# Kernel optimization log

Hardware: AMD Instinct MI355X
Metric: run time of the kernel (lower is better)

## Reference

```python
import jax, jax.numpy as jnp
import numpy as np

DIM = 512
HEADS = 8
HEAD = DIM // HEADS
T = 243          # temporal length, fixed by get_temporal_mask(243, ...)
N_JOINTS = 17    # skeleton joints
BATCH = 4        # number of clips; leading dim of x is BATCH*T
WINDOWS = (9, 27, 81, 243)  # temporal_MoE_type


def _temporal_masks():
    # Block-diagonal window masks: 0 inside each window block, -100000 outside,
    # exactly matching get_temporal_mask + torch.where(matrix == 0, -100000, 0).
    idx = np.arange(T)
    masks = np.stack([
        np.where((idx[:, None] // w) == (idx[None, :] // w), 0.0, -100000.0)
        for w in WINDOWS
    ]).astype(np.float32)  # (E, T, T)
    return jnp.asarray(masks)


def setup_inputs() -> dict:
    key = jax.random.key(0)
    k0, k1, k2, k3 = jax.random.split(key, 4)
    scaled = lambda k, shape, fan: jax.random.normal(k, shape, jnp.float32) * (fan ** -0.5)
    return {
        "x": jax.random.normal(k0, (BATCH * T, N_JOINTS, DIM), jnp.float32),
        "qkv_w": scaled(k1, (DIM, 3 * DIM), DIM),          # qkv (no bias, qkv_bias=False)
        "proj_w": scaled(k2, (DIM, DIM), DIM),             # output projection
        "proj_b": jnp.zeros((DIM,), jnp.float32),
        "te_w": scaled(k3, (DIM, len(WINDOWS)), DIM),      # temporal_expert_linear
        "te_b": jnp.zeros((len(WINDOWS),), jnp.float32),
        "seqlen": T,
    }


def reference(x, qkv_w, proj_w, proj_b, te_w, te_b, seqlen):
    BT, n, C = x.shape              # (b*T, N, C)
    b = BT // seqlen
    scale = HEAD ** -0.5
    # qkv projection -> q,k,v each (b, H, N, T, head_dim)
    qkv = (x @ qkv_w).reshape(b, seqlen, n, 3, HEADS, HEAD)
    qkv = jnp.transpose(qkv, (3, 0, 4, 2, 1, 5))  # (3, b, H, N, T, c)
    q, k, v = qkv[0], qkv[1], qkv[2]
    # temporal attention logits, shared across experts: (b, H, N, T, T)
    attn = jnp.einsum('bhntc,bhnsc->bhnts', q, k) * scale
    masks = _temporal_masks()                       # (E, T, T)
    attn = attn[None] + masks[:, None, None, None]  # (E, b, H, N, T, T)
    attn = jax.nn.softmax(attn, axis=-1)            # attn_drop is identity (p=0 / eval)
    eo = jnp.einsum('ebhnts,bhnsc->ebhntc', attn, v)
    E = masks.shape[0]
    # (E,b,H,N,T,c) -> (E,b,T,N,H,c) -> (E, b*T, N, C), matching permute(0,3,2,1,4)
    eo = jnp.transpose(eo, (0, 1, 4, 3, 2, 5)).reshape(E, BT, n, C)
    # expert gating: softmax(temporal_expert_linear(x)) over experts, per token
    w = jax.nn.softmax(x @ te_w + te_b, axis=-1)    # (BT, N, E)
    out = jnp.einsum('ebnc,bne->bnc', eo, w)        # fused expert recombination
    out = out @ proj_w + proj_b                     # proj (proj_drop identity)
    return out
```

## Files before the change

kernel.cpp:

```cpp
#include <hip/hip_runtime.h>
#include <hip/hip_bf16.h>
#include <cstdint>

#define TT 243
#define NJ 17
#define NB 4
#define NH 8
#define HD 64
#define CDIM 512
#define NROWS (NB*TT*NJ)
#define NBHN (NB*NH*NJ)

typedef unsigned short u16;
typedef __attribute__((ext_vector_type(8))) short short8;
typedef __attribute__((ext_vector_type(4))) float f32x4;

#define MFMA16(a, b, c) __builtin_amdgcn_mfma_f32_16x16x32_bf16((a), (b), (c), 0, 0, 0)
#define QSCALE 0.18033688011112042f

__device__ __forceinline__ void gl_lds16(const void* g, void* l) {
  __builtin_amdgcn_global_load_lds(
      (const __attribute__((address_space(1))) void*)g,
      (__attribute__((address_space(3))) void*)l, 16, 0, 0);
}

__device__ __forceinline__ u16 f2bf(float f) {
  union { float f; unsigned u; } v; v.f = f;
  unsigned r = v.u + 0x7FFFu + ((v.u >> 16) & 1u);
  return (u16)(r >> 16);
}

__device__ __forceinline__ float fast_exp2(float x) {
#if __has_builtin(__builtin_amdgcn_exp2f)
  return __builtin_amdgcn_exp2f(x);
#else
  return exp2f(x);
#endif
}
__device__ __forceinline__ float fast_rcp(float x) {
#if __has_builtin(__builtin_amdgcn_rcpf)
  return __builtin_amdgcn_rcpf(x);
#else
  return 1.f / x;
#endif
}
__device__ __forceinline__ unsigned pk_bf16(float a, float b) {
#if __has_builtin(__builtin_amdgcn_cvt_pk_bf16_f32)
  auto pk = __builtin_amdgcn_cvt_pk_bf16_f32(a, b);
  unsigned u; __builtin_memcpy(&u, &pk, sizeof(u));
  return u;
#else
  return (unsigned)f2bf(a) | ((unsigned)f2bf(b) << 16);
#endif
}

__device__ __forceinline__ float wave_reduce_sum(float v) {
#pragma unroll
  for (int off = 32; off > 0; off >>= 1) v += __shfl_xor(v, off, 64);
  return v;
}

#define CG_BLOCKS ((NROWS + 3) / 4)
#define T1_NB 48
#define T1_BLOCKS (48 * 16)
#define T2_NB 16
#define T2_BLOCKS (16 * 16)

__device__ __forceinline__ void trans_body(const float* __restrict__ in,
                                           u16* __restrict__ out, int K, int N,
                                           int nb, int kb, float (*tile)[33]) {
  int n0 = nb * 32, k0 = kb * 32;
  int tx = threadIdx.x & 31, ty = threadIdx.x >> 5;
#pragma unroll
  for (int p = 0; p < 4; ++p)
    tile[ty + p * 8][tx] = in[(size_t)(k0 + ty + p * 8) * N + n0 + tx];
  __syncthreads();
#pragma unroll
  for (int p = 0; p < 4; ++p)
    out[(size_t)(n0 + ty + p * 8) * K + k0 + tx] = f2bf(tile[tx][ty + p * 8]);
}

__global__ __launch_bounds__(256) void prep_kernel(
    const float* __restrict__ x, const float* __restrict__ te_w,
    const float* __restrict__ te_b, const float* __restrict__ qkv_w,
    const float* __restrict__ proj_w, u16* __restrict__ xb,
    float* __restrict__ gates, u16* __restrict__ wt, u16* __restrict__ pwt) {
  __shared__ float tile[32][33];
  int bid = blockIdx.x;
  if (bid >= CG_BLOCKS) {
    int r = bid - CG_BLOCKS;
    if (r < T1_BLOCKS) trans_body(qkv_w, wt, 512, 1536, r % T1_NB, r / T1_NB, tile);
    else {
      r -= T1_BLOCKS;
      trans_body(proj_w, pwt, 512, 512, r % T2_NB, r / T2_NB, tile);
    }
    return;
  }
  int w = threadIdx.x >> 6, l = threadIdx.x & 63;
  int row = bid * 4 + w;
  if (row >= NROWS) return;
  const float* xr = x + (size_t)row * CDIM;
  u16* xo = xb + (size_t)row * CDIM;
  float a0 = 0.f, a1 = 0.f, a2 = 0.f, a3 = 0.f;
#pragma unroll
  for (int p = 0; p < 2; ++p) {
    int c = (p * 64 + l) * 4;
    float4 v = *(const float4*)(xr + c);
    uint2 o;
    o.x = pk_bf16(v.x, v.y);
    o.y = pk_bf16(v.z, v.w);
    *(uint2*)(xo + c) = o;
    float xv[4] = {v.x, v.y, v.z, v.w};
#pragma unroll
    for (int q = 0; q < 4; ++q) {
      float4 wv = *(const float4*)(te_w + (size_t)(c + q) * 4);
      a0 += xv[q] * wv.x; a1 += xv[q] * wv.y;
      a2 += xv[q] * wv.z; a3 += xv[q] * wv.w;
    }
  }
  a0 = wave_reduce_sum(a0);
  a1 = wave_reduce_sum(a1);
  a2 = wave_reduce_sum(a2);
  a3 = wave_reduce_sum(a3);
  a0 += te_b[0]; a1 += te_b[1]; a2 += te_b[2]; a3 += te_b[3];
  float mx = fmaxf(fmaxf(a0, a1), fmaxf(a2, a3));
  float e0 = __expf(a0 - mx), e1 = __expf(a1 - mx);
  float e2 = __expf(a2 - mx), e3 = __expf(a3 - mx);
  float inv = fast_rcp(e0 + e1 + e2 + e3);
  if (l == 0) {
    *(float4*)(gates + (size_t)row * 4) =
        make_float4(e0 * inv, e1 * inv, e2 * inv, e3 * inv);
  }
}

__global__ __launch_bounds__(256) void qkv_gemm(
    const u16* __restrict__ xb, const u16* __restrict__ wt,
    u16* __restrict__ qh, u16* __restrict__ kh, u16* __restrict__ vb) {
  __shared__ u16 S[16640];
  u16* Al = S;
  u16* Bl = S + 8192;
  int tid = threadIdx.x;
  int w = tid >> 6;
  int c16 = tid & 15, g4 = (tid >> 4) & 3;
  int r0 = blockIdx.y * 128, n0 = blockIdx.x * 128;
  int wm = w & 1, wn = w >> 1;

  int rA = tid >> 3;
  int c8off = (((tid & 7) ^ (rA & 7)) * 8);
  size_t arow4[4], brow4[4];
#pragma unroll
  for (int it = 0; it < 4; ++it) {
    int m = r0 + it * 32 + rA;
    if (m >= NROWS) m = NROWS - 1;
    int bj = m / 243, t = m - bj * 243;
    int b = bj / 17, j = bj - b * 17;
    arow4[it] = ((size_t)(b * 243 + t) * 17 + j) * 512;
    brow4[it] = (size_t)(n0 + it * 32 + rA) * 512;
  }

  f32x4 acc[4][4] = {};
  for (int k0 = 0; k0 < CDIM; k0 += 64) {
    __syncthreads();
#pragma unroll
    for (int it = 0; it < 4; ++it) {
      gl_lds16(xb + arow4[it] + k0 + c8off, Al + (size_t)(it * 256 + (w * 64)) * 8);
      gl_lds16(wt + brow4[it] + k0 + c8off, Bl + (size_t)(it * 256 + (w * 64)) * 8);
    }
    __syncthreads();
    short8 af[4][2], bf[4][2];
#pragma unroll
    for (int i = 0; i < 4; ++i) {
      int rowa = wm * 64 + i * 16 + c16;
#pragma unroll
      for (int hh = 0; hh < 2; ++hh)
        af[i][hh] = *(const short8*)(Al + rowa * 64 + (((hh * 4 + g4) ^ (c16 & 7)) * 8));
    }
#pragma unroll
    for (int j = 0; j < 4; ++j) {
      int rowb = wn * 64 + j * 16 + c16;
#pragma unroll
      for (int hh = 0; hh < 2; ++hh)
        bf[j][hh] = *(const short8*)(Bl + rowb * 64 + (((hh * 4 + g4) ^ (c16 & 7)) * 8));
    }
#pragma unroll
    for (int i = 0; i < 4; ++i)
#pragma unroll
      for (int j = 0; j < 4; ++j) {
        acc[i][j] = MFMA16(af[i][0], bf[j][0], acc[i][j]);
        acc[i][j] = MFMA16(af[i][1], bf[j][1], acc[i][j]);
      }
  }

  if (n0 < 1024) {
#pragma unroll
    for (int i = 0; i < 4; ++i)
#pragma unroll
      for (int r = 0; r < 4; ++r) {
        int m = r0 + wm * 64 + i * 16 + g4 * 4 + r;
        if (m >= NROWS) continue;
        int bj = m / 243, t = m - bj * 243;
        int b = bj / 17, j = bj - b * 17;
#pragma unroll
        for (int jt = 0; jt < 4; ++jt) {
          int col = n0 + wn * 64 + jt * 16 + c16;
          int sel = col >> 9, h = (col >> 6) & 7, c = col & 63;
          u16* dst = sel ? kh : qh;
          float val = acc[i][jt][r];
          if (!sel) val *= QSCALE;
          dst[((size_t)((b * 8 + h) * 17 + j) * 243 + t) * 64 + c] = f2bf(val);
        }
      }
  } else {
    __syncthreads();
#pragma unroll
    for (int i = 0; i < 4; ++i)
#pragma unroll
      for (int jt = 0; jt < 4; ++jt)
#pragma unroll
        for (int r = 0; r < 4; ++r) {
          int row = wm * 64 + i * 16 + g4 * 4 + r;
          int colI = wn * 64 + jt * 16 + c16;
          S[colI * 130 + row] = f2bf(acc[i][jt][r]);
        }
    __syncthreads();
    int l = tid & 63;
    int hb = (n0 - 1024) >> 6;
    int m0 = r0 + 2 * l;
    int m1 = m0 + 1;
    bool v0 = m0 < NROWS, v1 = m1 < NROWS;
    int bj0 = m0 / 243, t0 = m0 - bj0 * 243;
    int b0 = bj0 / 17, j0 = bj0 - b0 * 17;
    int bj1 = m1 / 243, t1 = m1 - bj1 * 243;
    int b1 = bj1 / 17, j1 = bj1 - b1 * 17;
    size_t base0 = ((size_t)(b0 * 136 + j0) * 64) * 256 + t0;
    size_t base1 = ((size_t)(b1 * 136 + j1) * 64) * 256 + t1;
#pragma unroll 8
    for (int cc = 0; cc < 32; ++cc) {
      int colI = w * 32 + cc;
      int h = hb + (colI >> 6), c = colI & 63;
      ushort2 u = *(const ushort2*)&S[colI * 130 + 2 * l];
      size_t hoff = ((size_t)h * 17 * 64) * 256 + (size_t)c * 256;
      if (v0) vb[base0 + hoff] = u.x;
      if (v1) vb[base1 + hoff] = u.y;
    }
  }
}

__global__ __launch_bounds__(256, 4) void attn_kernel(
    const u16* __restrict__ qh, const u16* __restrict__ kh,
    const u16* __restrict__ vb, const float* __restrict__ gates,
    u16* __restrict__ preb) {
  __shared__ u16 L[16384];
  int bhn = blockIdx.x;
  int q0 = blockIdx.y * 64;
  int b = bhn / (NH * NJ);
  int hj = bhn - b * (NH * NJ);
  int h = hj / NJ, j = hj - h * NJ;
  int tid = threadIdx.x;
  int w = tid >> 6;
  int c16 = tid & 15, g4 = (tid >> 4) & 3;
  const u16* Kp = kh + (size_t)bhn * (TT * HD);
  const u16* Qp = qh + (size_t)bhn * (TT * HD);
  const u16* Vp = vb + (size_t)bhn * (HD * 256);
  u16* Rw = L + w * 4096;

#pragma unroll
  for (int it = 0; it < 8; ++it) {
    int F = it * 256 + tid;
    int s = F >> 3;
    int c8 = (F & 7) ^ (s & 7);
    int sg = s < TT ? s : TT - 1;
    gl_lds16(Kp + (size_t)sg * 64 + c8 * 8, L + (size_t)(it * 256 + (tid & ~63)) * 8);
  }
  __syncthreads();

  int tt = q0 + w * 16 + c16;
  bool tvalid = tt < TT;
  int tg = tvalid ? tt : TT - 1;

  short8 bq[2];
#pragma unroll
  for (int hh = 0; hh < 2; ++hh)
    bq[hh] = *(const short8*)(Qp + (size_t)tg * 64 + hh * 32 + g4 * 8);

  f32x4 acc[16];
#pragma unroll
  for (int st = 0; st < 16; ++st) acc[st] = (f32x4)(0.f);
#pragma unroll
  for (int st = 0; st < 16; ++st) {
    int sf = st * 16 + c16;
#pragma unroll
    for (int hh = 0; hh < 2; ++hh) {
      short8 ak = *(const short8*)(L + sf * 64 + ((hh * 4 + g4) ^ (sf & 7)) * 8);
      acc[st] = MFMA16(ak, bq[hh], acc[st]);
    }
  }
  __syncthreads();

#pragma unroll
  for (int r = 0; r < 4; ++r) {
    int s = 240 + g4 * 4 + r;
    if (s >= TT) acc[15][r] = -1e30f;
  }
  float M = -1e30f;
#pragma unroll
  for (int st = 0; st < 16; ++st)
#pragma unroll
    for (int r = 0; r < 4; ++r) M = fmaxf(M, acc[st][r]);
  M = fmaxf(M, __shfl_xor(M, 16, 64));
  M = fmaxf(M, __shfl_xor(M, 32, 64));

#pragma unroll
  for (int st = 0; st < 16; ++st)
#pragma unroll
    for (int r = 0; r < 4; ++r) acc[st][r] = fast_exp2(acc[st][r] - M);

  int t9b = (tg / 9) * 9;
  int t27b = (tg / 27) * 27;
  int t81b = (tg / 81) * 81;
  float l9 = 0.f, l27 = 0.f, l81 = 0.f, l243 = 0.f;
#pragma unroll
  for (int st = 0; st < 16; ++st)
#pragma unroll
    for (int r = 0; r < 4; ++r) {
      int s = st * 16 + g4 * 4 + r;
      float e = acc[st][r];
      l243 += e;
      l81 += ((unsigned)(s - t81b) < 81u) ? e : 0.f;
      l27 += ((unsigned)(s - t27b) < 27u) ? e : 0.f;
      l9  += ((unsigned)(s - t9b)  <  9u) ? e : 0.f;
    }
  l9   += __shfl_xor(l9, 16, 64);   l9   += __shfl_xor(l9, 32, 64);
  l27  += __shfl_xor(l27, 16, 64);  l27  += __shfl_xor(l27, 32, 64);
  l81  += __shfl_xor(l81, 16, 64);  l81  += __shfl_xor(l81, 32, 64);
  l243 += __shfl_xor(l243, 16, 64); l243 += __shfl_xor(l243, 32, 64);

  float4 gv = *(const float4*)(gates + ((size_t)(b * TT + tg) * NJ + j) * 4);
  float gam3 = gv.w * fast_rcp(l243);
  float gam2 = gam3 + gv.z * fast_rcp(l81);
  float gam1 = gam2 + gv.y * fast_rcp(l27);
  float gam0 = gam1 + gv.x * fast_rcp(l9);

#pragma unroll
  for (int st = 0; st < 16; ++st) {
    float rv[4];
#pragma unroll
    for (int r = 0; r < 4; ++r) {
      int s = st * 16 + g4 * 4 + r;
      float e = acc[st][r];
      float cw = ((unsigned)(s - t9b) < 9u) ? gam0
               : ((unsigned)(s - t27b) < 27u) ? gam1
               : ((unsigned)(s - t81b) < 81u) ? gam2 : gam3;
      rv[r] = tvalid ? e * cw : 0.f;
    }
    uint2 pk;
    pk.x = pk_bf16(rv[0], rv[1]);
    pk.y = pk_bf16(rv[2], rv[3]);
    int c8 = st * 2 + (g4 >> 1);
    int slot = (c8 & 24) | ((c8 & 7) ^ (c16 & 7));
    *(uint2*)(Rw + c16 * 256 + slot * 8 + (g4 & 1) * 4) = pk;
  }

  short8 ar[8];
#pragma unroll
  for (int h2 = 0; h2 < 8; ++h2) {
    int cc = h2 * 4 + g4;
    int slot = (cc & 24) | ((cc & 7) ^ (c16 & 7));
    ar[h2] = *(const short8*)(Rw + c16 * 256 + slot * 8);
  }
#pragma unroll
  for (int jt = 0; jt < 4; ++jt) {
    int c = jt * 16 + c16;
    f32x4 o = (f32x4)(0.f);
#pragma unroll
    for (int h2 = 0; h2 < 8; ++h2) {
      short8 bv = *(const short8*)(Vp + (size_t)c * 256 + h2 * 32 + g4 * 8);
      o = MFMA16(ar[h2], bv, o);
    }
#pragma unroll
    for (int r = 0; r < 4; ++r) {
      int t = q0 + w * 16 + g4 * 4 + r;
      if (t < TT)
        preb[((size_t)(b * TT + t) * NJ + j) * 512 + h * 64 + c] = f2bf(o[r]);
    }
  }
}

__global__ __launch_bounds__(256) void proj_gemm(
    const u16* __restrict__ preb, const u16* __restrict__ pwt,
    const float* __restrict__ bias, float* __restrict__ out) {
  __shared__ u16 Al[8192];
  __shared__ u16 Bl[8192];
  int tid = threadIdx.x;
  int w = tid >> 6;
  int c16 = tid & 15, g4 = (tid >> 4) & 3;
  int r0 = blockIdx.y * 128, n0 = blockIdx.x * 128;
  int wm = w & 1, wn = w >> 1;

  int rA = tid >> 3;
  int c8off = (((tid & 7) ^ (rA & 7)) * 8);
  size_t arow4[4], brow4[4];
#pragma unroll
  for (int it = 0; it < 4; ++it) {
    int m = r0 + it * 32 + rA;
    if (m >= NROWS) m = NROWS - 1;
    arow4[it] = (size_t)m * 512;
    brow4[it] = (size_t)(n0 + it * 32 + rA) * 512;
  }

  f32x4 acc[4][4] = {};
  for (int k0 = 0; k0 < CDIM; k0 += 64) {
    __syncthreads();
#pragma unroll
    for (int it = 0; it < 4; ++it) {
      gl_lds16(preb + arow4[it] + k0 + c8off, Al + (size_t)(it * 256 + (w * 64)) * 8);
      gl_lds16(pwt + brow4[it] + k0 + c8off, Bl + (size_t)(it * 256 + (w * 64)) * 8);
    }
    __syncthreads();
    short8 af[4][2], bf[4][2];
#pragma unroll
    for (int i = 0; i < 4; ++i) {
      int rowa = wm * 64 + i * 16 + c16;
#pragma unroll
      for (int hh = 0; hh < 2; ++hh)
        af[i][hh] = *(const short8*)(Al + rowa * 64 + (((hh * 4 + g4) ^ (c16 & 7)) * 8));
    }
#pragma unroll
    for (int j = 0; j < 4; ++j) {
      int rowb = wn * 64 + j * 16 + c16;
#pragma unroll
      for (int hh = 0; hh < 2; ++hh)
        bf[j][hh] = *(const short8*)(Bl + rowb * 64 + (((hh * 4 + g4) ^ (c16 & 7)) * 8));
    }
#pragma unroll
    for (int i = 0; i < 4; ++i)
#pragma unroll
      for (int j = 0; j < 4; ++j) {
        acc[i][j] = MFMA16(af[i][0], bf[j][0], acc[i][j]);
        acc[i][j] = MFMA16(af[i][1], bf[j][1], acc[i][j]);
      }
  }
#pragma unroll
  for (int i = 0; i < 4; ++i)
#pragma unroll
    for (int r = 0; r < 4; ++r) {
      int row = r0 + wm * 64 + i * 16 + g4 * 4 + r;
      if (row >= NROWS) continue;
#pragma unroll
      for (int jt = 0; jt < 4; ++jt) {
        int col = n0 + wn * 64 + jt * 16 + c16;
        out[(size_t)row * 512 + col] = acc[i][jt][r] + bias[col];
      }
    }
}

extern "C" void kernel_launch(void* const* d_in, const int* in_sizes, int n_in,
                              void* d_out, int out_size, void* d_ws, size_t ws_size,
                              hipStream_t stream) {
  (void)in_sizes; (void)n_in; (void)out_size; (void)ws_size;
  const float* x      = (const float*)d_in[0];
  const float* qkv_w  = (const float*)d_in[1];
  const float* proj_w = (const float*)d_in[2];
  const float* proj_b = (const float*)d_in[3];
  const float* te_w   = (const float*)d_in[4];
  const float* te_b   = (const float*)d_in[5];

  char* p = (char*)d_ws;
  auto alloc = [&](size_t bytes) {
    void* r = (void*)p;
    p += (bytes + 255) & ~(size_t)255;
    return r;
  };
  u16*   xb    = (u16*)alloc((size_t)NROWS * 512 * 2);
  u16*   wt    = (u16*)alloc((size_t)1536 * 512 * 2);
  u16*   pwt   = (u16*)alloc((size_t)512 * 512 * 2);
  float* gates = (float*)alloc((size_t)NROWS * 4 * 4);
  u16*   qhb   = (u16*)alloc((size_t)NBHN * 243 * 64 * 2);
  u16*   khb   = (u16*)alloc((size_t)NBHN * 243 * 64 * 2);
  u16*   vb    = (u16*)alloc((size_t)NBHN * 64 * 256 * 2);
  u16*   preb  = (u16*)alloc((size_t)NROWS * 512 * 2);
  float* out   = (float*)d_out;

  hipLaunchKernelGGL(prep_kernel, dim3(CG_BLOCKS + T1_BLOCKS + T2_BLOCKS), dim3(256),
                     0, stream, x, te_w, te_b, qkv_w, proj_w, xb, gates, wt, pwt);
  hipLaunchKernelGGL(qkv_gemm, dim3(12, (NROWS + 127) / 128), dim3(256), 0, stream,
                     xb, wt, qhb, khb, vb);
  hipLaunchKernelGGL(attn_kernel, dim3(NBHN, 4), dim3(256), 0, stream,
                     qhb, khb, vb, gates, preb);
  hipLaunchKernelGGL(proj_gemm, dim3(4, (NROWS + 127) / 128), dim3(256), 0, stream,
                     preb, pwt, proj_b, out);
}
```

Measured before the change: 213.5 us.

## Fuse x bf16 conversion and expert gating into QKV GEMM

Removes the separate pass that converts x to bf16 and computes the gating softmax. The QKV GEMM now loads fp32 x directly, converts it in registers and writes it into LDS, and an extra column of blocks computes the gate logits with MFMA against a transposed bf16 te_w. The attention softmax sums are restructured to accumulate in vectors, and the invalid-row masking is folded into the gamma coefficients. In exchange, every GEMM block re-reads fp32 x, which doubles its A-side traffic and loses the async LDS loads, and the gate logits are now computed in bf16.

```diff
diff --git a/kernel.cpp b/kernel.cpp
--- a/kernel.cpp
+++ b/kernel.cpp
@@ -54,13 +54,6 @@
 #endif
 }
 
-__device__ __forceinline__ float wave_reduce_sum(float v) {
-#pragma unroll
-  for (int off = 32; off > 0; off >>= 1) v += __shfl_xor(v, off, 64);
-  return v;
-}
-
-#define CG_BLOCKS ((NROWS + 3) / 4)
 #define T1_NB 48
 #define T1_BLOCKS (48 * 16)
 #define T2_NB 16
@@ -81,73 +74,43 @@
 }
 
 __global__ __launch_bounds__(256) void prep_kernel(
-    const float* __restrict__ x, const float* __restrict__ te_w,
-    const float* __restrict__ te_b, const float* __restrict__ qkv_w,
-    const float* __restrict__ proj_w, u16* __restrict__ xb,
-    float* __restrict__ gates, u16* __restrict__ wt, u16* __restrict__ pwt) {
+    const float* __restrict__ qkv_w, const float* __restrict__ proj_w,
+    const float* __restrict__ te_w, u16* __restrict__ wt,
+    u16* __restrict__ pwt, u16* __restrict__ tewt) {
   __shared__ float tile[32][33];
   int bid = blockIdx.x;
-  if (bid >= CG_BLOCKS) {
-    int r = bid - CG_BLOCKS;
-    if (r < T1_BLOCKS) trans_body(qkv_w, wt, 512, 1536, r % T1_NB, r / T1_NB, tile);
-    else {
-      r -= T1_BLOCKS;
-      trans_body(proj_w, pwt, 512, 512, r % T2_NB, r / T2_NB, tile);
-    }
-    return;
-  }
-  int w = threadIdx.x >> 6, l = threadIdx.x & 63;
-  int row = bid * 4 + w;
-  if (row >= NROWS) return;
-  const float* xr = x + (size_t)row * CDIM;
-  u16* xo = xb + (size_t)row * CDIM;
-  float a0 = 0.f, a1 = 0.f, a2 = 0.f, a3 = 0.f;
-#pragma unroll
-  for (int p = 0; p < 2; ++p) {
-    int c = (p * 64 + l) * 4;
-    float4 v = *(const float4*)(xr + c);
-    uint2 o;
-    o.x = pk_bf16(v.x, v.y);
-    o.y = pk_bf16(v.z, v.w);
-    *(uint2*)(xo + c) = o;
-    float xv[4] = {v.x, v.y, v.z, v.w};
-#pragma unroll
-    for (int q = 0; q < 4; ++q) {
-      float4 wv = *(const float4*)(te_w + (size_t)(c + q) * 4);
-      a0 += xv[q] * wv.x; a1 += xv[q] * wv.y;
-      a2 += xv[q] * wv.z; a3 += xv[q] * wv.w;
-    }
-  }
-  a0 = wave_reduce_sum(a0);
-  a1 = wave_reduce_sum(a1);
-  a2 = wave_reduce_sum(a2);
-  a3 = wave_reduce_sum(a3);
-  a0 += te_b[0]; a1 += te_b[1]; a2 += te_b[2]; a3 += te_b[3];
-  float mx = fmaxf(fmaxf(a0, a1), fmaxf(a2, a3));
-  float e0 = __expf(a0 - mx), e1 = __expf(a1 - mx);
-  float e2 = __expf(a2 - mx), e3 = __expf(a3 - mx);
-  float inv = fast_rcp(e0 + e1 + e2 + e3);
-  if (l == 0) {
-    *(float4*)(gates + (size_t)row * 4) =
-        make_float4(e0 * inv, e1 * inv, e2 * inv, e3 * inv);
+  if (bid < T1_BLOCKS) {
+    trans_body(qkv_w, wt, 512, 1536, bid % T1_NB, bid / T1_NB, tile);
+  } else if (bid < T1_BLOCKS + T2_BLOCKS) {
+    int r = bid - T1_BLOCKS;
+    trans_body(proj_w, pwt, 512, 512, r % T2_NB, r / T2_NB, tile);
+  } else {
+#pragma unroll
+    for (int i = 0; i < 8; ++i) {
+      int idx = threadIdx.x + i * 256;
+      int e = idx >> 9, c = idx & 511;
+      tewt[idx] = f2bf(te_w[(size_t)c * 4 + e]);
+    }
   }
 }
 
 __global__ __launch_bounds__(256) void qkv_gemm(
-    const u16* __restrict__ xb, const u16* __restrict__ wt,
-    u16* __restrict__ qh, u16* __restrict__ kh, u16* __restrict__ vb) {
+    const float* __restrict__ xf, const u16* __restrict__ wt,
+    const u16* __restrict__ tewt, const float* __restrict__ te_b,
+    u16* __restrict__ qh, u16* __restrict__ kh, u16* __restrict__ vb,
+    float* __restrict__ gates) {
   __shared__ u16 S[16640];
   u16* Al = S;
   u16* Bl = S + 8192;
   int tid = threadIdx.x;
   int w = tid >> 6;
   int c16 = tid & 15, g4 = (tid >> 4) & 3;
-  int r0 = blockIdx.y * 128, n0 = blockIdx.x * 128;
-  int wm = w & 1, wn = w >> 1;
-
+  int r0 = blockIdx.y * 128;
+  int bx = blockIdx.x;
   int rA = tid >> 3;
-  int c8off = (((tid & 7) ^ (rA & 7)) * 8);
-  size_t arow4[4], brow4[4];
+  int c8e = (((tid & 7) ^ (rA & 7)) * 8);
+
+  size_t arow4[4];
 #pragma unroll
   for (int it = 0; it < 4; ++it) {
     int m = r0 + it * 32 + rA;
@@ -155,16 +118,97 @@
     int bj = m / 243, t = m - bj * 243;
     int b = bj / 17, j = bj - b * 17;
     arow4[it] = ((size_t)(b * 243 + t) * 17 + j) * 512;
+  }
+
+  if (bx == 12) {
+    u16* Tl = Bl;
+    *(uint2*)(Tl + tid * 4) = make_uint2(0u, 0u);
+    f32x4 gacc[2] = {};
+    for (int k0 = 0; k0 < CDIM; k0 += 64) {
+      __syncthreads();
+      float4 fa[4][2];
+#pragma unroll
+      for (int it = 0; it < 4; ++it) {
+        const float* src = xf + arow4[it] + k0 + c8e;
+        fa[it][0] = *(const float4*)(src);
+        fa[it][1] = *(const float4*)(src + 4);
+      }
+#pragma unroll
+      for (int it = 0; it < 4; ++it) {
+        uint4 pkv;
+        pkv.x = pk_bf16(fa[it][0].x, fa[it][0].y);
+        pkv.y = pk_bf16(fa[it][0].z, fa[it][0].w);
+        pkv.z = pk_bf16(fa[it][1].x, fa[it][1].y);
+        pkv.w = pk_bf16(fa[it][1].z, fa[it][1].w);
+        *(uint4*)(Al + (size_t)(it * 256 + tid) * 8) = pkv;
+      }
+      if (tid < 32) {
+        int row = tid >> 3;
+        gl_lds16(tewt + (size_t)row * 512 + k0 + (((tid & 7) ^ row) * 8), Tl);
+      }
+      __syncthreads();
+      short8 tf[2];
+#pragma unroll
+      for (int hh = 0; hh < 2; ++hh)
+        tf[hh] = *(const short8*)(Tl + c16 * 64 + (((hh * 4 + g4) ^ (c16 & 7)) * 8));
+#pragma unroll
+      for (int i2 = 0; i2 < 2; ++i2) {
+        int rowa = w * 32 + i2 * 16 + c16;
+#pragma unroll
+        for (int hh = 0; hh < 2; ++hh) {
+          short8 af = *(const short8*)(Al + rowa * 64 + (((hh * 4 + g4) ^ (c16 & 7)) * 8));
+          gacc[i2] = MFMA16(af, tf[hh], gacc[i2]);
+        }
+      }
+    }
+    float bias = (c16 < 4) ? te_b[c16 & 3] : 0.f;
+#pragma unroll
+    for (int i2 = 0; i2 < 2; ++i2)
+#pragma unroll
+      for (int r = 0; r < 4; ++r) {
+        int m = r0 + w * 32 + i2 * 16 + g4 * 4 + r;
+        if (m >= NROWS) continue;
+        float v = gacc[i2][r] + bias;
+        float mx = fmaxf(v, __shfl_xor(v, 1, 64));
+        mx = fmaxf(mx, __shfl_xor(mx, 2, 64));
+        float e = __expf(v - mx);
+        float sum = e + __shfl_xor(e, 1, 64);
+        sum += __shfl_xor(sum, 2, 64);
+        if (c16 < 4) {
+          int bj = m / 243, t = m - bj * 243;
+          int b = bj / 17, j = bj - b * 17;
+          gates[((size_t)(b * 243 + t) * 17 + j) * 4 + c16] = e * fast_rcp(sum);
+        }
+      }
+    return;
+  }
+
+  int n0 = bx * 128;
+  int wm = w & 1, wn = w >> 1;
+  size_t brow4[4];
+#pragma unroll
+  for (int it = 0; it < 4; ++it)
     brow4[it] = (size_t)(n0 + it * 32 + rA) * 512;
-  }
 
   f32x4 acc[4][4] = {};
   for (int k0 = 0; k0 < CDIM; k0 += 64) {
     __syncthreads();
+    float4 fa[4][2];
 #pragma unroll
     for (int it = 0; it < 4; ++it) {
-      gl_lds16(xb + arow4[it] + k0 + c8off, Al + (size_t)(it * 256 + (w * 64)) * 8);
-      gl_lds16(wt + brow4[it] + k0 + c8off, Bl + (size_t)(it * 256 + (w * 64)) * 8);
+      const float* src = xf + arow4[it] + k0 + c8e;
+      fa[it][0] = *(const float4*)(src);
+      fa[it][1] = *(const float4*)(src + 4);
+    }
+#pragma unroll
+    for (int it = 0; it < 4; ++it) {
+      gl_lds16(wt + brow4[it] + k0 + c8e, Bl + (size_t)(it * 256 + (w * 64)) * 8);
+      uint4 pkv;
+      pkv.x = pk_bf16(fa[it][0].x, fa[it][0].y);
+      pkv.y = pk_bf16(fa[it][0].z, fa[it][0].w);
+      pkv.z = pk_bf16(fa[it][1].x, fa[it][1].y);
+      pkv.w = pk_bf16(fa[it][1].z, fa[it][1].w);
+      *(uint4*)(Al + (size_t)(it * 256 + tid) * 8) = pkv;
     }
     __syncthreads();
     short8 af[4][2], bf[4][2];
@@ -318,18 +362,24 @@
   int t9b = (tg / 9) * 9;
   int t27b = (tg / 27) * 27;
   int t81b = (tg / 81) * 81;
-  float l9 = 0.f, l27 = 0.f, l81 = 0.f, l243 = 0.f;
+  f32x4 vall = acc[0];
+#pragma unroll
+  for (int st = 1; st < 16; ++st) vall += acc[st];
+  float l243 = (vall[0] + vall[1]) + (vall[2] + vall[3]);
+  f32x4 v81 = (f32x4)(0.f), v27 = (f32x4)(0.f), v9 = (f32x4)(0.f);
 #pragma unroll
   for (int st = 0; st < 16; ++st)
 #pragma unroll
     for (int r = 0; r < 4; ++r) {
       int s = st * 16 + g4 * 4 + r;
       float e = acc[st][r];
-      l243 += e;
-      l81 += ((unsigned)(s - t81b) < 81u) ? e : 0.f;
-      l27 += ((unsigned)(s - t27b) < 27u) ? e : 0.f;
-      l9  += ((unsigned)(s - t9b)  <  9u) ? e : 0.f;
-    }
+      v81[r] += ((unsigned)(s - t81b) < 81u) ? e : 0.f;
+      v27[r] += ((unsigned)(s - t27b) < 27u) ? e : 0.f;
+      v9[r]  += ((unsigned)(s - t9b)  <  9u) ? e : 0.f;
+    }
+  float l81 = (v81[0] + v81[1]) + (v81[2] + v81[3]);
+  float l27 = (v27[0] + v27[1]) + (v27[2] + v27[3]);
+  float l9  = (v9[0] + v9[1]) + (v9[2] + v9[3]);
   l9   += __shfl_xor(l9, 16, 64);   l9   += __shfl_xor(l9, 32, 64);
   l27  += __shfl_xor(l27, 16, 64);  l27  += __shfl_xor(l27, 32, 64);
   l81  += __shfl_xor(l81, 16, 64);  l81  += __shfl_xor(l81, 32, 64);
@@ -340,6 +390,7 @@
   float gam2 = gam3 + gv.z * fast_rcp(l81);
   float gam1 = gam2 + gv.y * fast_rcp(l27);
   float gam0 = gam1 + gv.x * fast_rcp(l9);
+  if (!tvalid) { gam0 = 0.f; gam1 = 0.f; gam2 = 0.f; gam3 = 0.f; }
 
 #pragma unroll
   for (int st = 0; st < 16; ++st) {
@@ -351,7 +402,7 @@
       float cw = ((unsigned)(s - t9b) < 9u) ? gam0
                : ((unsigned)(s - t27b) < 27u) ? gam1
                : ((unsigned)(s - t81b) < 81u) ? gam2 : gam3;
-      rv[r] = tvalid ? e * cw : 0.f;
+      rv[r] = e * cw;
     }
     uint2 pk;
     pk.x = pk_bf16(rv[0], rv[1]);
@@ -471,9 +522,9 @@
     p += (bytes + 255) & ~(size_t)255;
     return r;
   };
-  u16*   xb    = (u16*)alloc((size_t)NROWS * 512 * 2);
   u16*   wt    = (u16*)alloc((size_t)1536 * 512 * 2);
   u16*   pwt   = (u16*)alloc((size_t)512 * 512 * 2);
+  u16*   tewt  = (u16*)alloc((size_t)4 * 512 * 2);
   float* gates = (float*)alloc((size_t)NROWS * 4 * 4);
   u16*   qhb   = (u16*)alloc((size_t)NBHN * 243 * 64 * 2);
   u16*   khb   = (u16*)alloc((size_t)NBHN * 243 * 64 * 2);
@@ -481,10 +532,10 @@
   u16*   preb  = (u16*)alloc((size_t)NROWS * 512 * 2);
   float* out   = (float*)d_out;
 
-  hipLaunchKernelGGL(prep_kernel, dim3(CG_BLOCKS + T1_BLOCKS + T2_BLOCKS), dim3(256),
-                     0, stream, x, te_w, te_b, qkv_w, proj_w, xb, gates, wt, pwt);
-  hipLaunchKernelGGL(qkv_gemm, dim3(12, (NROWS + 127) / 128), dim3(256), 0, stream,
-                     xb, wt, qhb, khb, vb);
+  hipLaunchKernelGGL(prep_kernel, dim3(T1_BLOCKS + T2_BLOCKS + 1), dim3(256), 0, stream,
+                     qkv_w, proj_w, te_w, wt, pwt, tewt);
+  hipLaunchKernelGGL(qkv_gemm, dim3(13, (NROWS + 127) / 128), dim3(256), 0, stream,
+                     x, wt, tewt, te_b, qhb, khb, vb, gates);
   hipLaunchKernelGGL(attn_kernel, dim3(NBHN, 4), dim3(256), 0, stream,
                      qhb, khb, vb, gates, preb);
   hipLaunchKernelGGL(proj_gemm, dim3(4, (NROWS + 127) / 128), dim3(256), 0, stream,
```

New measurement: 227.8 us. 6.7% more time.

## Remap GEMM blocks XCD-aware and vectorize softmax window sums

Applied to the files above, without the earlier changes.

Both GEMMs now launch a 1D grid, and each block index is remapped so that consecutive work tiles land on the same XCD (bid&7 spread). The aim is better L2 reuse of A and B tiles on the multi-die MI355X. In the attention kernel, the per-window exp sums are accumulated as 4-wide vectors to break serial dependency chains. The invalid-row masking moves from per-element selects to zeroing the gate coefficients once. The remap hardcodes the tile counts (1560 and 520), so it depends on NROWS being fixed.

```diff
diff --git a/kernel.cpp b/kernel.cpp
--- a/kernel.cpp
+++ b/kernel.cpp
@@ -142,7 +142,10 @@
   int tid = threadIdx.x;
   int w = tid >> 6;
   int c16 = tid & 15, g4 = (tid >> 4) & 3;
-  int r0 = blockIdx.y * 128, n0 = blockIdx.x * 128;
+  int bid = blockIdx.x;
+  int wrk = (bid & 7) * 195 + (bid >> 3);
+  int r0 = (wrk / 12) * 128;
+  int n0 = (wrk % 12) * 128;
   int wm = w & 1, wn = w >> 1;
 
   int rA = tid >> 3;
@@ -318,18 +321,24 @@
   int t9b = (tg / 9) * 9;
   int t27b = (tg / 27) * 27;
   int t81b = (tg / 81) * 81;
-  float l9 = 0.f, l27 = 0.f, l81 = 0.f, l243 = 0.f;
+  f32x4 vall = acc[0];
+#pragma unroll
+  for (int st = 1; st < 16; ++st) vall += acc[st];
+  float l243 = (vall[0] + vall[1]) + (vall[2] + vall[3]);
+  f32x4 v81 = (f32x4)(0.f), v27 = (f32x4)(0.f), v9 = (f32x4)(0.f);
 #pragma unroll
   for (int st = 0; st < 16; ++st)
 #pragma unroll
     for (int r = 0; r < 4; ++r) {
       int s = st * 16 + g4 * 4 + r;
       float e = acc[st][r];
-      l243 += e;
-      l81 += ((unsigned)(s - t81b) < 81u) ? e : 0.f;
-      l27 += ((unsigned)(s - t27b) < 27u) ? e : 0.f;
-      l9  += ((unsigned)(s - t9b)  <  9u) ? e : 0.f;
-    }
+      v81[r] += ((unsigned)(s - t81b) < 81u) ? e : 0.f;
+      v27[r] += ((unsigned)(s - t27b) < 27u) ? e : 0.f;
+      v9[r]  += ((unsigned)(s - t9b)  <  9u) ? e : 0.f;
+    }
+  float l81 = (v81[0] + v81[1]) + (v81[2] + v81[3]);
+  float l27 = (v27[0] + v27[1]) + (v27[2] + v27[3]);
+  float l9  = (v9[0] + v9[1]) + (v9[2] + v9[3]);
   l9   += __shfl_xor(l9, 16, 64);   l9   += __shfl_xor(l9, 32, 64);
   l27  += __shfl_xor(l27, 16, 64);  l27  += __shfl_xor(l27, 32, 64);
   l81  += __shfl_xor(l81, 16, 64);  l81  += __shfl_xor(l81, 32, 64);
@@ -340,6 +349,7 @@
   float gam2 = gam3 + gv.z * fast_rcp(l81);
   float gam1 = gam2 + gv.y * fast_rcp(l27);
   float gam0 = gam1 + gv.x * fast_rcp(l9);
+  if (!tvalid) { gam0 = 0.f; gam1 = 0.f; gam2 = 0.f; gam3 = 0.f; }
 
 #pragma unroll
   for (int st = 0; st < 16; ++st) {
@@ -351,7 +361,7 @@
       float cw = ((unsigned)(s - t9b) < 9u) ? gam0
                : ((unsigned)(s - t27b) < 27u) ? gam1
                : ((unsigned)(s - t81b) < 81u) ? gam2 : gam3;
-      rv[r] = tvalid ? e * cw : 0.f;
+      rv[r] = e * cw;
     }
     uint2 pk;
     pk.x = pk_bf16(rv[0], rv[1]);
@@ -394,7 +404,10 @@
   int tid = threadIdx.x;
   int w = tid >> 6;
   int c16 = tid & 15, g4 = (tid >> 4) & 3;
-  int r0 = blockIdx.y * 128, n0 = blockIdx.x * 128;
+  int bid = blockIdx.x;
+  int wrk = (bid & 7) * 65 + (bid >> 3);
+  int r0 = (wrk >> 2) * 128;
+  int n0 = (wrk & 3) * 128;
   int wm = w & 1, wn = w >> 1;
 
   int rA = tid >> 3;
@@ -483,10 +496,10 @@
 
   hipLaunchKernelGGL(prep_kernel, dim3(CG_BLOCKS + T1_BLOCKS + T2_BLOCKS), dim3(256),
                      0, stream, x, te_w, te_b, qkv_w, proj_w, xb, gates, wt, pwt);
-  hipLaunchKernelGGL(qkv_gemm, dim3(12, (NROWS + 127) / 128), dim3(256), 0, stream,
+  hipLaunchKernelGGL(qkv_gemm, dim3(1560), dim3(256), 0, stream,
                      xb, wt, qhb, khb, vb);
   hipLaunchKernelGGL(attn_kernel, dim3(NBHN, 4), dim3(256), 0, stream,
                      qhb, khb, vb, gates, preb);
-  hipLaunchKernelGGL(proj_gemm, dim3(4, (NROWS + 127) / 128), dim3(256), 0, stream,
+  hipLaunchKernelGGL(proj_gemm, dim3(520), dim3(256), 0, stream,
                      preb, pwt, proj_b, out);
 }
```

Result: no change. 212.6 us (-0.4%).
